# Optimization experiments

Hardware: AMD Instinct MI355X
Metric: run time of the kernel (lower is better)

The kernel has to match this reference:

```python
import jax, jax.numpy as jnp
import numpy as np

B = 1024
IN_SIZE = 8192
OUT_SIZE = 8192
CONNECTIVITY = 32
NNZ = OUT_SIZE * CONNECTIVITY  # 262144


def setup_inputs() -> dict:
    key = jax.random.key(0)
    kx, kv, ki = jax.random.split(key, 3)
    x = jax.random.normal(kx, (B, IN_SIZE), dtype=jnp.float32)
    # uniform init as in module: (rand-0.5)*2*sqrt(3/connectivity)
    scale = np.sqrt(3.0 / CONNECTIVITY)
    values = (jax.random.uniform(kv, (NNZ,), dtype=jnp.float32) - 0.5) * 2.0 * scale
    # indices_out = list(range(out_size)) * connectivity -> arange(nnz) % out_size
    idx_out = (jnp.arange(NNZ) % OUT_SIZE).astype(jnp.int32)
    # uniform distribution: randperm(nnz) % in_size ~ uniform over [0, in_size)
    idx_in = jax.random.randint(ki, (NNZ,), 0, IN_SIZE, dtype=jnp.int32)
    return {"x": x, "values": values, "idx_out": idx_out, "idx_in": idx_in,
            "out_size": OUT_SIZE}


def reference(x, values, idx_out, idx_in, out_size):
    # y[b, o] = sum over nnz k with idx_out[k]==o of values[k] * x[b, idx_in[k]]
    # (spmm(indices, values, out, in, x.T).T in the original)
    contrib = x[:, idx_in] * values[None, :]          # [B, nnz]
    y = jnp.zeros((x.shape[0], out_size), dtype=x.dtype)
    y = y.at[:, idx_out].add(contrib)                 # scatter-add over output rows
    return y
```

## Files before the change

### kernel.cpp

```cpp
#include <hip/hip_runtime.h>

#define IN_SIZE   8192
#define OUT_SIZE  8192
#define CONN      32
#define NNZ       (OUT_SIZE * CONN)
#define BATCH     1024
#define BT        8
#define OT        4096
#define NTHREADS  1024
#define OPT       (OT / NTHREADS)

typedef int          int4v   __attribute__((ext_vector_type(4)));
typedef float        float2v __attribute__((ext_vector_type(2)));
typedef float        float4v __attribute__((ext_vector_type(4)));
typedef unsigned int uint4v  __attribute__((ext_vector_type(4)));

__device__ __forceinline__ unsigned bf16rne(float f) {
  unsigned u = __builtin_bit_cast(unsigned, f);
  return (u + 0x7fffu + ((u >> 16) & 1u)) >> 16;
}

__global__ __launch_bounds__(256)
void pack_kernel(const float* __restrict__ values,
                 const int*   __restrict__ idx_in,
                 unsigned int* __restrict__ pk) {
  int k = blockIdx.x * 256 + threadIdx.x;
  if (k < NNZ) {
    unsigned u = __builtin_bit_cast(unsigned, values[k]);
    unsigned r = (u + 0xFFFu + ((u >> 13) & 1u)) >> 13;
    unsigned i = (unsigned)idx_in[k];
    unsigned s = ((i & 3u) << 11) | (i >> 2);
    pk[k] = (s << 19) | (r & 0x7FFFFu);
  }
}

template<bool PACKED>
__global__ __launch_bounds__(NTHREADS, 4)
void spl_kernel(const float* __restrict__ x,
                const unsigned int* __restrict__ pk,
                const float* __restrict__ values,
                const int* __restrict__ idx_in,
                float* __restrict__ y) {
  __shared__ uint4v xs[IN_SIZE];

  const int bid = blockIdx.x;
  const int oh  = bid >> 7;
  const int bb  = bid & 127;
  const int b0  = bb * BT;
  const int t   = threadIdx.x;
  const int o0  = oh * OT + t * OPT;

  #pragma unroll
  for (int p = 0; p < IN_SIZE / (NTHREADS * 4); ++p) {
    int c4 = p * NTHREADS + t;
    float4v r[BT];
    #pragma unroll
    for (int b = 0; b < BT; ++b)
      r[b] = *(const float4v*)(x + (size_t)(b0 + b) * IN_SIZE + c4 * 4);
    #pragma unroll
    for (int q = 0; q < 4; ++q) {
      uint4v w;
      w.x = bf16rne(r[0][q]) | (bf16rne(r[1][q]) << 16);
      w.y = bf16rne(r[2][q]) | (bf16rne(r[3][q]) << 16);
      w.z = bf16rne(r[4][q]) | (bf16rne(r[5][q]) << 16);
      w.w = bf16rne(r[6][q]) | (bf16rne(r[7][q]) << 16);
      xs[q * 2048 + c4] = w;
    }
  }
  __syncthreads();

  if constexpr (PACKED) {
    float2v acc2[OPT][4];
    #pragma unroll
    for (int q = 0; q < OPT; ++q)
      #pragma unroll
      for (int c = 0; c < 4; ++c) acc2[q][c] = (float2v){0.0f, 0.0f};

    const char* xsb = (const char*)xs;

#define LDPK(J)  (*(const uint4v*)(pk + (J) * OUT_SIZE + o0))
#define GATHER(G, P)                                                        \
    {                                                                       \
      _Pragma("unroll")                                                     \
      for (int q = 0; q < OPT; ++q)                                         \
        G[q] = *(const uint4v*)(xsb + ((P[q] >> 15) & 0x1FFF0u));           \
    }
#define CONSUME(P, G)                                                       \
    {                                                                       \
      _Pragma("unroll")                                                     \
      for (int q = 0; q < OPT; ++q) {                                       \
        float v = __builtin_bit_cast(float, P[q] << 13);                    \
        float2v v2 = {v, v};                                                \
        _Pragma("unroll")                                                   \
        for (int c = 0; c < 4; ++c) {                                       \
          float2v xp = {__builtin_bit_cast(float, G[q][c] << 16),           \
                        __builtin_bit_cast(float, G[q][c] & 0xFFFF0000u)};  \
          acc2[q][c] += v2 * xp;                                            \
        }                                                                   \
      }                                                                     \
    }

    uint4v pk0 = LDPK(0);
    uint4v pk1 = LDPK(1);
    uint4v g0[OPT];
    GATHER(g0, pk0);

    #pragma unroll
    for (int j = 0; j < CONN; j += 2) {
      uint4v pk2 = LDPK(j + 2 < CONN ? j + 2 : 0);
      uint4v g1[OPT];
      GATHER(g1, pk1);
      CONSUME(pk0, g0);
      uint4v pk3 = LDPK(j + 3 < CONN ? j + 3 : 0);
      uint4v g2[OPT];
      GATHER(g2, pk2);
      CONSUME(pk1, g1);
      pk0 = pk2; pk1 = pk3;
      #pragma unroll
      for (int q = 0; q < OPT; ++q) g0[q] = g2[q];
    }
#undef LDPK
#undef GATHER
#undef CONSUME

    #pragma unroll
    for (int bt = 0; bt < BT; ++bt) {
      float* yr = y + (size_t)(b0 + bt) * OUT_SIZE + o0;
      const int c = bt >> 1, h = bt & 1;
      float4v w = {acc2[0][c][h], acc2[1][c][h], acc2[2][c][h], acc2[3][c][h]};
      __builtin_nontemporal_store(w, (float4v*)yr);
    }
  } else {
    float acc[OPT][BT];
    #pragma unroll
    for (int q = 0; q < OPT; ++q)
      #pragma unroll
      for (int bt = 0; bt < BT; ++bt) acc[q][bt] = 0.0f;
    const char* xsb = (const char*)xs;
    for (int j = 0; j < CONN; ++j) {
      const int kb = j * OUT_SIZE + o0;
      int4v i0 = *(const int4v*)(idx_in + kb);
      float4v v0 = *(const float4v*)(values + kb);
      #pragma unroll
      for (int q = 0; q < OPT; ++q) {
        unsigned i = (unsigned)i0[q];
        unsigned s = ((i & 3u) << 11) | (i >> 2);
        float v = v0[q];
        uint4v gv = *(const uint4v*)(xsb + (s << 4));
        acc[q][0] += v * __builtin_bit_cast(float, gv.x << 16);
        acc[q][1] += v * __builtin_bit_cast(float, gv.x & 0xFFFF0000u);
        acc[q][2] += v * __builtin_bit_cast(float, gv.y << 16);
        acc[q][3] += v * __builtin_bit_cast(float, gv.y & 0xFFFF0000u);
        acc[q][4] += v * __builtin_bit_cast(float, gv.z << 16);
        acc[q][5] += v * __builtin_bit_cast(float, gv.z & 0xFFFF0000u);
        acc[q][6] += v * __builtin_bit_cast(float, gv.w << 16);
        acc[q][7] += v * __builtin_bit_cast(float, gv.w & 0xFFFF0000u);
      }
    }
    #pragma unroll
    for (int bt = 0; bt < BT; ++bt) {
      float* yr = y + (size_t)(b0 + bt) * OUT_SIZE + o0;
      float4v w = {acc[0][bt], acc[1][bt], acc[2][bt], acc[3][bt]};
      __builtin_nontemporal_store(w, (float4v*)yr);
    }
  }
}

extern "C" void kernel_launch(void* const* d_in, const int* in_sizes, int n_in,
                              void* d_out, int out_size, void* d_ws, size_t ws_size,
                              hipStream_t stream) {
  const float* x      = (const float*)d_in[0];
  const float* values = (const float*)d_in[1];
  const int*   idx_in = (const int*)d_in[3];
  float*       y      = (float*)d_out;

  const dim3 grid((BATCH / BT) * (OUT_SIZE / OT));
  const dim3 blk(NTHREADS);

  if (ws_size >= (size_t)NNZ * sizeof(unsigned int)) {
    unsigned int* pk = (unsigned int*)d_ws;
    hipLaunchKernelGGL(pack_kernel, dim3(NNZ / 256), dim3(256), 0, stream,
                       values, idx_in, pk);
    hipLaunchKernelGGL((spl_kernel<true>), grid, blk, 0, stream,
                       x, pk, values, idx_in, y);
  } else {
    hipLaunchKernelGGL((spl_kernel<false>), grid, blk, 0, stream,
                       x, nullptr, values, idx_in, y);
  }
}
```

Before: 32.78 us.

## Reorder per-output nonzeros in pack kernel to spread LDS gathers across banks

The pack kernel now runs one thread per output column. Each thread counting-sorts that column's 32 nonzeros by a 3-bit field of the input index, then rotates the order by the column's lane group so that concurrent lanes gather from different LDS bank groups at each step. The goal is to reduce LDS bank conflicts in the main kernel's gather loop. The cost is a pack kernel with far fewer threads (8192) that each do serial work, which may lengthen the preprocessing stage.

```diff
diff --git a/kernel.cpp b/kernel.cpp
--- a/kernel.cpp
+++ b/kernel.cpp
@@ -24,13 +24,38 @@
 void pack_kernel(const float* __restrict__ values,
                  const int*   __restrict__ idx_in,
                  unsigned int* __restrict__ pk) {
-  int k = blockIdx.x * 256 + threadIdx.x;
-  if (k < NNZ) {
-    unsigned u = __builtin_bit_cast(unsigned, values[k]);
+  const int o = blockIdx.x * 256 + threadIdx.x;
+  const unsigned c = (unsigned)((o >> 2) & 7);
+
+  int idx[CONN];
+  unsigned cl = 0, ch = 0;
+  #pragma unroll
+  for (int j = 0; j < CONN; ++j) {
+    idx[j] = idx_in[j * OUT_SIZE + o];
+    unsigned oct = ((unsigned)idx[j] >> 2) & 7u;
+    if (oct < 4u) cl += 1u << (oct * 8u);
+    else          ch += 1u << ((oct - 4u) * 8u);
+  }
+  unsigned n0 = cl & 255u, n1 = (cl >> 8) & 255u, n2 = (cl >> 16) & 255u, n3 = cl >> 24;
+  unsigned n4 = ch & 255u, n5 = (ch >> 8) & 255u, n6 = (ch >> 16) & 255u;
+  unsigned p1 = n0, p2 = p1 + n1, p3 = p2 + n2, p4 = p3 + n3;
+  unsigned p5 = p4 + n4, p6 = p5 + n5, p7 = p6 + n6;
+  unsigned pl = (p1 << 8) | (p2 << 16) | (p3 << 24);
+  unsigned ph = p4 | (p5 << 8) | (p6 << 16) | (p7 << 24);
+
+  #pragma unroll
+  for (int j = 0; j < CONN; ++j) {
+    unsigned i = (unsigned)idx[j];
+    unsigned oct = (i >> 2) & 7u;
+    unsigned sh = (oct & 3u) * 8u;
+    unsigned s;
+    if (oct < 4u) { s = (pl >> sh) & 255u; pl += 1u << sh; }
+    else          { s = (ph >> sh) & 255u; ph += 1u << sh; }
+    unsigned jp = (s + 32u - 4u * c) & 31u;
+    unsigned u = __builtin_bit_cast(unsigned, values[j * OUT_SIZE + o]);
     unsigned r = (u + 0xFFFu + ((u >> 13) & 1u)) >> 13;
-    unsigned i = (unsigned)idx_in[k];
-    unsigned s = ((i & 3u) << 11) | (i >> 2);
-    pk[k] = (s << 19) | (r & 0x7FFFFu);
+    unsigned swz = ((i & 3u) << 11) | (i >> 2);
+    pk[jp * OUT_SIZE + o] = (swz << 19) | (r & 0x7FFFFu);
   }
 }
 
@@ -179,7 +204,7 @@
 
   if (ws_size >= (size_t)NNZ * sizeof(unsigned int)) {
     unsigned int* pk = (unsigned int*)d_ws;
-    hipLaunchKernelGGL(pack_kernel, dim3(NNZ / 256), dim3(256), 0, stream,
+    hipLaunchKernelGGL(pack_kernel, dim3(OUT_SIZE / 256), dim3(256), 0, stream,
                        values, idx_in, pk);
     hipLaunchKernelGGL((spl_kernel<true>), grid, blk, 0, stream,
                        x, pk, values, idx_in, y);
```

Result: slower. 43.54 us (+32.8%).
